# Kernel tuning notes

Hardware: AMD Instinct MI355X
Metric: run time of the kernel (lower is better)

Reference implementation:

```python
import jax, jax.numpy as jnp
import numpy as np

N, E = 10000, 640000
IN_FT, OUT_FT = 512, 128
NEG_SLOPE = 0.2


def setup_inputs() -> dict:
    key = jax.random.key(0)
    ks = jax.random.split(key, 10)
    seq = jax.random.normal(ks[0], (N, IN_FT), dtype=jnp.float32)
    # edges with no self-loops: dst = (src + offset) % N, offset in [1, N-1]
    src = jax.random.randint(ks[1], (E,), 0, N)
    off = jax.random.randint(ks[2], (E,), 1, N)
    dst = (src + off) % N
    edge_index = jnp.stack([src, dst]).astype(jnp.int64)
    # parameters (xavier-ish scale)
    W_fc = jax.random.normal(ks[3], (OUT_FT, IN_FT), dtype=jnp.float32) * (1.0 / np.sqrt(IN_FT))
    W_gat = jax.random.normal(ks[4], (OUT_FT, OUT_FT), dtype=jnp.float32) * (1.0 / np.sqrt(OUT_FT))
    att_src = jax.random.normal(ks[5], (OUT_FT,), dtype=jnp.float32) * 0.1
    att_dst = jax.random.normal(ks[6], (OUT_FT,), dtype=jnp.float32) * 0.1
    gat_bias = jnp.zeros((OUT_FT,), dtype=jnp.float32)
    bias = jnp.zeros((OUT_FT,), dtype=jnp.float32)
    prelu_a = jnp.asarray(0.25, dtype=jnp.float32)
    return {"seq": seq, "edge_index": edge_index, "W_fc": W_fc, "W_gat": W_gat,
            "att_src": att_src, "att_dst": att_dst, "gat_bias": gat_bias,
            "bias": bias, "prelu_a": prelu_a}


def _gat_forward(seq, src, dst, W_fc, W_gat, att_src, att_dst, gat_bias, bias, prelu_a):
    n = seq.shape[0]
    x = seq @ W_fc.T                      # [N, out_ft] fc (no bias)
    h = x @ W_gat.T                       # GATConv internal linear (no bias)
    a_s = h @ att_src                     # [N] per-node src attention logits
    a_d = h @ att_dst                     # [N]
    e = a_s[src] + a_d[dst]               # [E'] per-edge raw score
    e = jnp.where(e >= 0, e, NEG_SLOPE * e)
    # segment softmax over destination node
    m = jax.ops.segment_max(e, dst, num_segments=n)
    m = jnp.where(jnp.isfinite(m), m, 0.0)
    p = jnp.exp(e - m[dst])
    denom = jax.ops.segment_sum(p, dst, num_segments=n)
    alpha = p / (denom[dst] + 1e-16)
    msgs = alpha[:, None] * h[src]        # [E', out_ft]
    out = jax.ops.segment_sum(msgs, dst, num_segments=n) + gat_bias
    out = out + bias
    return jnp.where(out >= 0, out, prelu_a * out)  # PReLU


def reference(seq, edge_index, W_fc, W_gat, att_src, att_dst, gat_bias, bias, prelu_a):
    n = seq.shape[0]
    loops = jnp.arange(n, dtype=edge_index.dtype)   # add_self_loops
    src = jnp.concatenate([edge_index[0], loops])
    dst = jnp.concatenate([edge_index[1], loops])
    return _gat_forward(seq, src, dst, W_fc, W_gat, att_src, att_dst, gat_bias, bias, prelu_a)
```

## Files before the change

kernel.cpp:

```cpp
#include <hip/hip_runtime.h>
#include <hip/hip_bf16.h>

#define IN_FT 512
#define OUT_FT 128
#define NEG_SLOPE 0.2f
#define SHIFT_C 4.0f
#define CAPB 1440
#define NBMAX 1024

typedef __attribute__((ext_vector_type(8))) short short8;
typedef __attribute__((ext_vector_type(4))) short short4v;
typedef __attribute__((ext_vector_type(4))) float float4v;

__device__ inline short f2bf_s(float x) {
    __hip_bfloat16 b = __float2bfloat16(x);
    union { __hip_bfloat16 b; short s; } u;
    u.b = b;
    return u.s;
}
__device__ inline float bf2f(short s) {
    union { float f; unsigned u; } u;
    u.u = ((unsigned)(unsigned short)s) << 16;
    return u.f;
}

__global__ void k_prep(const float* __restrict__ Wg,
                       const float* __restrict__ Wf,
                       short* __restrict__ whf,
                       int* __restrict__ gcur, int nb) {
    if (blockIdx.x >= 256) {
        int i = (blockIdx.x - 256) * 256 + threadIdx.x;
        if (i < nb) gcur[i] = 0;
        return;
    }
    int idx = blockIdx.x * blockDim.x + threadIdx.x;
    int o = idx >> 9;
    int k = idx & 511;
    float s = 0.f;
#pragma unroll 8
    for (int j = 0; j < OUT_FT; ++j)
        s += Wg[o * OUT_FT + j] * Wf[j * IN_FT + k];
    int t = o >> 4, l15 = o & 15;
    int kc = k >> 5, q = (k >> 3) & 3, jj = k & 7;
    whf[(((kc * 8 + t) * 64) + q * 16 + l15) * 8 + jj] = f2bf_s(s);
}

__launch_bounds__(256)
__global__ void k_main(const float* __restrict__ seq,
                       const short8* __restrict__ whf,
                       const float* __restrict__ att_s_v,
                       const float* __restrict__ att_d_v,
                       short* __restrict__ h16,
                       float* __restrict__ a_s,
                       float* __restrict__ a_d,
                       const int* __restrict__ src,
                       const int* __restrict__ dstv,
                       int* __restrict__ gcur,
                       unsigned* __restrict__ bins,
                       int N, int E, int nb, int GB) {
    __shared__ char smem[24576];
    if (blockIdx.x >= GB) {
        int* hist  = (int*)smem;
        int* sbase = hist + NBMAX;
        int* scur  = sbase + NBMAX;
        int e0 = (blockIdx.x - GB) * 2048;
        for (int t = threadIdx.x; t < nb; t += 256) hist[t] = 0;
        __syncthreads();
        int myd[8];
#pragma unroll
        for (int k = 0; k < 8; ++k) {
            int e = e0 + k * 256 + threadIdx.x;
            myd[k] = (e < E) ? dstv[e] : -1;
            if ((unsigned)myd[k] < (unsigned)N) atomicAdd(&hist[myd[k] >> 4], 1);
            else myd[k] = -1;
        }
        __syncthreads();
        for (int t = threadIdx.x; t < nb; t += 256) {
            int c = hist[t];
            sbase[t] = c ? atomicAdd(&gcur[t], c) : 0;
            scur[t] = 0;
        }
        __syncthreads();
#pragma unroll
        for (int k = 0; k < 8; ++k) {
            if (myd[k] >= 0) {
                int e = e0 + k * 256 + threadIdx.x;
                int b = myd[k] >> 4;
                int slot = sbase[b] + atomicAdd(&scur[b], 1);
                if (slot < CAPB) {
                    int s = src[e];
                    if ((unsigned)s >= (unsigned)N) s = 0;
                    bins[(size_t)b * CAPB + slot] = ((unsigned)s << 4) | (myd[k] & 15);
                }
            }
        }
        return;
    }
    short* As = (short*)smem;
    float4v* red = (float4v*)smem;

    int wave = threadIdx.x >> 6;
    int lane = threadIdx.x & 63;
    int l15 = lane & 15, quad = lane >> 4;
    int rows0 = blockIdx.x * 16;

#pragma unroll
    for (int i = 0; i < 8; ++i) {
        int idx = threadIdx.x + 256 * i;
        int r = idx >> 7, c4 = idx & 127;
        int row = rows0 + r;
        int rowc = row < N ? row : N - 1;
        float4 v = *(const float4*)(seq + (size_t)rowc * IN_FT + c4 * 4);
        short4v b;
        b[0] = f2bf_s(v.x); b[1] = f2bf_s(v.y); b[2] = f2bf_s(v.z); b[3] = f2bf_s(v.w);
        int kc = c4 >> 3, q = (c4 >> 1) & 3, half = c4 & 1;
        *(short4v*)(As + (((kc * 4 + q) * 16 + r) * 8 + half * 4)) = b;
    }
    __syncthreads();

    float4v acc[8];
    for (int t = 0; t < 8; ++t) acc[t] = (float4v){0.f, 0.f, 0.f, 0.f};

#pragma unroll
    for (int kk = 0; kk < 4; ++kk) {
        int kc = wave * 4 + kk;
        short8 a = *(const short8*)(As + ((kc * 4 + quad) * 16 + l15) * 8);
        const short8* bhp = whf + (size_t)kc * 512 + lane;
#pragma unroll
        for (int t = 0; t < 8; ++t) {
            short8 bh = bhp[t * 64];
            acc[t] = __builtin_amdgcn_mfma_f32_16x16x32_bf16(a, bh, acc[t], 0, 0, 0);
        }
    }
    __syncthreads();
    if (wave > 0) {
        float4v* base = red + ((wave - 1) * 8) * 64 + lane;
        for (int t = 0; t < 8; ++t) base[t * 64] = acc[t];
    }
    __syncthreads();
    if (wave != 0) return;
    for (int w2 = 0; w2 < 3; ++w2) {
        const float4v* base = red + (w2 * 8) * 64 + lane;
        for (int t = 0; t < 8; ++t) {
            float4v v = base[t * 64];
            acc[t][0] += v[0]; acc[t][1] += v[1]; acc[t][2] += v[2]; acc[t][3] += v[3];
        }
    }
    int rbase = rows0 + quad * 4;
    for (int r = 0; r < 4; ++r) {
        int rr = rbase + r;
        if (rr < N) {
            short* hr = h16 + (size_t)rr * OUT_FT;
            for (int t = 0; t < 8; ++t) hr[t * 16 + l15] = f2bf_s(acc[t][r]);
        }
    }
    float asv[8], adv[8];
    for (int t = 0; t < 8; ++t) {
        asv[t] = att_s_v[t * 16 + l15];
        adv[t] = att_d_v[t * 16 + l15];
    }
    for (int r = 0; r < 4; ++r) {
        float ps = 0.f, pd = 0.f;
        for (int t = 0; t < 8; ++t) {
            float v = acc[t][r];
            ps += v * asv[t];
            pd += v * adv[t];
        }
        for (int m = 1; m < 16; m <<= 1) {
            ps += __shfl_xor(ps, m);
            pd += __shfl_xor(pd, m);
        }
        int rr = rbase + r;
        if (l15 == 0 && rr < N) { a_s[rr] = ps; a_d[rr] = pd; }
    }
}

__launch_bounds__(256)
__global__ void k_agg(const short* __restrict__ h16, const float* __restrict__ a_s,
                      const float* __restrict__ a_d,
                      const int* __restrict__ gcur, const unsigned* __restrict__ bins,
                      const float* __restrict__ gat_bias,
                      const float* __restrict__ bias,
                      const float* __restrict__ prelu_a,
                      float* __restrict__ out, int N) {
    __shared__ int   srcs[CAPB];
    __shared__ float pvals[CAPB];
    __shared__ int   hist[16], base[16], cur16[16];
    __shared__ float ads[16];
    int b = blockIdx.x;
    int d0 = b << 4;
    int nd = N - d0; if (nd > 16) nd = 16;
    int tid = threadIdx.x;

    if (tid < 16) {
        hist[tid] = 0;
        ads[tid] = (tid < nd) ? a_d[d0 + tid] : 0.f;
    }
    __syncthreads();

    int cnt = gcur[b]; if (cnt > CAPB) cnt = CAPB;
    const unsigned* binp = bins + (size_t)b * CAPB;

    for (int c = tid; c < cnt; c += 256) atomicAdd(&hist[binp[c] & 15], 1);
    __syncthreads();
    if (tid == 0) {
        int run = 0;
        for (int i = 0; i < 16; ++i) { base[i] = run; run += hist[i]; cur16[i] = 0; }
    }
    __syncthreads();
    for (int c = tid; c < cnt; c += 256) {
        unsigned pk = binp[c];
        int dl = pk & 15, sv = pk >> 4;
        float ev = a_s[sv] + ads[dl];
        ev = (ev >= 0.f) ? ev : NEG_SLOPE * ev;
        float p = __expf(ev - SHIFT_C);
        int slot = base[dl] + atomicAdd(&cur16[dl], 1);
        srcs[slot] = sv;
        pvals[slot] = p;
    }
    __syncthreads();

    int w = tid >> 6, L = tid & 63;
    float b0 = gat_bias[2 * L] + bias[2 * L];
    float b1 = gat_bias[2 * L + 1] + bias[2 * L + 1];
    float pa = prelu_a[0];
    for (int dl = w; dl < nd; dl += 4) {
        int d = d0 + dl;
        float adi = ads[dl];
        float e0 = a_s[d] + adi;
        e0 = (e0 >= 0.f) ? e0 : NEG_SLOPE * e0;
        float p0 = __expf(e0 - SHIFT_C);
        short2 hs0 = *(const short2*)(h16 + (size_t)d * OUT_FT + 2 * L);
        float acc0 = p0 * bf2f(hs0.x), acc1 = p0 * bf2f(hs0.y);
        float dsum = 0.f;
        int beg = base[dl], n = hist[dl];
        for (int c = 0; c < n; c += 64) {
            int nv = n - c; if (nv > 64) nv = 64;
            int sv = 0; float pl = 0.f;
            if (L < nv) { sv = srcs[beg + c + L]; pl = pvals[beg + c + L]; }
            dsum += pl;
            int e = 0;
            for (; e + 16 <= nv; e += 16) {
#pragma unroll
                for (int k = 0; k < 16; ++k) {
                    float p = __shfl(pl, e + k);
                    int ss = __shfl(sv, e + k);
                    short2 hv = *(const short2*)(h16 + (size_t)ss * OUT_FT + 2 * L);
                    acc0 += p * bf2f(hv.x);
                    acc1 += p * bf2f(hv.y);
                }
            }
            for (; e < nv; ++e) {
                float p = __shfl(pl, e);
                int ss = __shfl(sv, e);
                short2 hv = *(const short2*)(h16 + (size_t)ss * OUT_FT + 2 * L);
                acc0 += p * bf2f(hv.x);
                acc1 += p * bf2f(hv.y);
            }
        }
        for (int m = 1; m < 64; m <<= 1) dsum += __shfl_xor(dsum, m);
        float inv = 1.f / (dsum + p0 + 1e-16f);
        float o0 = acc0 * inv + b0;
        float o1 = acc1 * inv + b1;
        o0 = (o0 >= 0.f) ? o0 : pa * o0;
        o1 = (o1 >= 0.f) ? o1 : pa * o1;
        float2 ov; ov.x = o0; ov.y = o1;
        *(float2*)(out + (size_t)d * OUT_FT + 2 * L) = ov;
    }
}

extern "C" void kernel_launch(void* const* d_in, const int* in_sizes, int n_in,
                              void* d_out, int out_size, void* d_ws, size_t ws_size,
                              hipStream_t stream) {
    const float* seq     = (const float*)d_in[0];
    const int*   ei      = (const int*)d_in[1];
    const float* W_fc    = (const float*)d_in[2];
    const float* W_gat   = (const float*)d_in[3];
    const float* att_src = (const float*)d_in[4];
    const float* att_dst = (const float*)d_in[5];
    const float* gat_b   = (const float*)d_in[6];
    const float* bias    = (const float*)d_in[7];
    const float* prelu_a = (const float*)d_in[8];

    int N = in_sizes[0] / IN_FT;
    int E = in_sizes[1] / 2;
    const int* src = ei;
    const int* dst = ei + E;
    int nb = (N + 15) >> 4;

    char* wsb = (char*)d_ws;
    size_t cur = 0;
    auto alloc = [&](size_t bytes) -> void* {
        void* p = (void*)(wsb + cur);
        cur += (bytes + 255) & ~(size_t)255;
        return p;
    };
    short*    h16  = (short*)alloc((size_t)N * OUT_FT * 2);
    float*    a_s  = (float*)alloc((size_t)N * 4);
    float*    a_d  = (float*)alloc((size_t)N * 4);
    int*      gcur = (int*)alloc((size_t)nb * 4);
    unsigned* bins = (unsigned*)alloc((size_t)nb * CAPB * 4);
    short*    whf  = (short*)alloc((size_t)OUT_FT * IN_FT * 2);

    int GB = (N + 15) / 16;
    int PB = (E + 2047) / 2048;

    k_prep<<<dim3(256 + (nb + 255) / 256), dim3(256), 0, stream>>>(W_gat, W_fc, whf, gcur, nb);
    k_main<<<dim3(GB + PB), dim3(256), 0, stream>>>(
        seq, (const short8*)whf, att_src, att_dst, h16, a_s, a_d,
        src, dst, gcur, bins, N, E, nb, GB);
    k_agg<<<dim3(nb), dim3(256), 0, stream>>>(
        h16, a_s, a_d, gcur, bins, gat_b, bias, prelu_a, (float*)d_out, N);
}
```

Measured before the change: 139.3 us.

## Shrink aggregation buckets to 8 destinations and gather h rows without shuffles

Destination buckets go from 16 to 8 nodes. That doubles the number of aggregation blocks and halves the shared-memory footprint per block. Sources and weights are packed into one int2 LDS array, and the inner loop reads them as a broadcast from LDS instead of using wave shuffles. The loop batches 8 gathers of h16 rows before accumulating, to expose memory-level parallelism. The gcur zeroing moves from an extra k_prep block range to hipMemsetAsync, which adds one stream operation.

```diff
diff --git a/kernel.cpp b/kernel.cpp
--- a/kernel.cpp
+++ b/kernel.cpp
@@ -5,8 +5,8 @@
 #define OUT_FT 128
 #define NEG_SLOPE 0.2f
 #define SHIFT_C 4.0f
-#define CAPB 1440
-#define NBMAX 1024
+#define CAP8 768
+#define NBMAX 1280
 
 typedef __attribute__((ext_vector_type(8))) short short8;
 typedef __attribute__((ext_vector_type(4))) short short4v;
@@ -26,13 +26,7 @@
 
 __global__ void k_prep(const float* __restrict__ Wg,
                        const float* __restrict__ Wf,
-                       short* __restrict__ whf,
-                       int* __restrict__ gcur, int nb) {
-    if (blockIdx.x >= 256) {
-        int i = (blockIdx.x - 256) * 256 + threadIdx.x;
-        if (i < nb) gcur[i] = 0;
-        return;
-    }
+                       short* __restrict__ whf) {
     int idx = blockIdx.x * blockDim.x + threadIdx.x;
     int o = idx >> 9;
     int k = idx & 511;
@@ -71,7 +65,7 @@
         for (int k = 0; k < 8; ++k) {
             int e = e0 + k * 256 + threadIdx.x;
             myd[k] = (e < E) ? dstv[e] : -1;
-            if ((unsigned)myd[k] < (unsigned)N) atomicAdd(&hist[myd[k] >> 4], 1);
+            if ((unsigned)myd[k] < (unsigned)N) atomicAdd(&hist[myd[k] >> 3], 1);
             else myd[k] = -1;
         }
         __syncthreads();
@@ -85,12 +79,12 @@
         for (int k = 0; k < 8; ++k) {
             if (myd[k] >= 0) {
                 int e = e0 + k * 256 + threadIdx.x;
-                int b = myd[k] >> 4;
+                int b = myd[k] >> 3;
                 int slot = sbase[b] + atomicAdd(&scur[b], 1);
-                if (slot < CAPB) {
+                if (slot < CAP8) {
                     int s = src[e];
                     if ((unsigned)s >= (unsigned)N) s = 0;
-                    bins[(size_t)b * CAPB + slot] = ((unsigned)s << 4) | (myd[k] & 15);
+                    bins[(size_t)b * CAP8 + slot] = ((unsigned)s << 3) | (myd[k] & 7);
                 }
             }
         }
@@ -183,40 +177,39 @@
                       const float* __restrict__ bias,
                       const float* __restrict__ prelu_a,
                       float* __restrict__ out, int N) {
-    __shared__ int   srcs[CAPB];
-    __shared__ float pvals[CAPB];
-    __shared__ int   hist[16], base[16], cur16[16];
-    __shared__ float ads[16];
+    __shared__ int2  spair[CAP8];
+    __shared__ int   hist[8], base[8], cur8[8];
+    __shared__ float ads[8];
     int b = blockIdx.x;
-    int d0 = b << 4;
-    int nd = N - d0; if (nd > 16) nd = 16;
+    int d0 = b << 3;
+    int nd = N - d0; if (nd > 8) nd = 8;
     int tid = threadIdx.x;
 
-    if (tid < 16) {
+    if (tid < 8) {
         hist[tid] = 0;
         ads[tid] = (tid < nd) ? a_d[d0 + tid] : 0.f;
     }
     __syncthreads();
 
-    int cnt = gcur[b]; if (cnt > CAPB) cnt = CAPB;
-    const unsigned* binp = bins + (size_t)b * CAPB;
-
-    for (int c = tid; c < cnt; c += 256) atomicAdd(&hist[binp[c] & 15], 1);
+    int cnt = gcur[b]; if (cnt > CAP8) cnt = CAP8;
+    const unsigned* binp = bins + (size_t)b * CAP8;
+
+    for (int c = tid; c < cnt; c += 256) atomicAdd(&hist[binp[c] & 7], 1);
     __syncthreads();
     if (tid == 0) {
         int run = 0;
-        for (int i = 0; i < 16; ++i) { base[i] = run; run += hist[i]; cur16[i] = 0; }
+        for (int i = 0; i < 8; ++i) { base[i] = run; run += hist[i]; cur8[i] = 0; }
     }
     __syncthreads();
     for (int c = tid; c < cnt; c += 256) {
         unsigned pk = binp[c];
-        int dl = pk & 15, sv = pk >> 4;
+        int dl = pk & 7, sv = pk >> 3;
         float ev = a_s[sv] + ads[dl];
         ev = (ev >= 0.f) ? ev : NEG_SLOPE * ev;
         float p = __expf(ev - SHIFT_C);
-        int slot = base[dl] + atomicAdd(&cur16[dl], 1);
-        srcs[slot] = sv;
-        pvals[slot] = p;
+        int slot = base[dl] + atomicAdd(&cur8[dl], 1);
+        int2 sp; sp.x = sv; sp.y = __float_as_int(p);
+        spair[slot] = sp;
     }
     __syncthreads();
 
@@ -234,31 +227,30 @@
         float acc0 = p0 * bf2f(hs0.x), acc1 = p0 * bf2f(hs0.y);
         float dsum = 0.f;
         int beg = base[dl], n = hist[dl];
-        for (int c = 0; c < n; c += 64) {
-            int nv = n - c; if (nv > 64) nv = 64;
-            int sv = 0; float pl = 0.f;
-            if (L < nv) { sv = srcs[beg + c + L]; pl = pvals[beg + c + L]; }
-            dsum += pl;
-            int e = 0;
-            for (; e + 16 <= nv; e += 16) {
-#pragma unroll
-                for (int k = 0; k < 16; ++k) {
-                    float p = __shfl(pl, e + k);
-                    int ss = __shfl(sv, e + k);
-                    short2 hv = *(const short2*)(h16 + (size_t)ss * OUT_FT + 2 * L);
-                    acc0 += p * bf2f(hv.x);
-                    acc1 += p * bf2f(hv.y);
-                }
+        int e = 0;
+        for (; e + 8 <= n; e += 8) {
+            float pp[8]; short2 hh[8];
+#pragma unroll
+            for (int j = 0; j < 8; ++j) {
+                int2 sp = spair[beg + e + j];
+                pp[j] = __int_as_float(sp.y);
+                hh[j] = *(const short2*)(h16 + (size_t)sp.x * OUT_FT + 2 * L);
             }
-            for (; e < nv; ++e) {
-                float p = __shfl(pl, e);
-                int ss = __shfl(sv, e);
-                short2 hv = *(const short2*)(h16 + (size_t)ss * OUT_FT + 2 * L);
-                acc0 += p * bf2f(hv.x);
-                acc1 += p * bf2f(hv.y);
+#pragma unroll
+            for (int j = 0; j < 8; ++j) {
+                dsum += pp[j];
+                acc0 += pp[j] * bf2f(hh[j].x);
+                acc1 += pp[j] * bf2f(hh[j].y);
             }
         }
-        for (int m = 1; m < 64; m <<= 1) dsum += __shfl_xor(dsum, m);
+        for (; e < n; ++e) {
+            int2 sp = spair[beg + e];
+            float p = __int_as_float(sp.y);
+            short2 hv = *(const short2*)(h16 + (size_t)sp.x * OUT_FT + 2 * L);
+            dsum += p;
+            acc0 += p * bf2f(hv.x);
+            acc1 += p * bf2f(hv.y);
+        }
         float inv = 1.f / (dsum + p0 + 1e-16f);
         float o0 = acc0 * inv + b0;
         float o1 = acc1 * inv + b1;
@@ -286,7 +278,7 @@
     int E = in_sizes[1] / 2;
     const int* src = ei;
     const int* dst = ei + E;
-    int nb = (N + 15) >> 4;
+    int nb = (N + 7) >> 3;
 
     char* wsb = (char*)d_ws;
     size_t cur = 0;
@@ -299,13 +291,14 @@
     float*    a_s  = (float*)alloc((size_t)N * 4);
     float*    a_d  = (float*)alloc((size_t)N * 4);
     int*      gcur = (int*)alloc((size_t)nb * 4);
-    unsigned* bins = (unsigned*)alloc((size_t)nb * CAPB * 4);
+    unsigned* bins = (unsigned*)alloc((size_t)nb * CAP8 * 4);
     short*    whf  = (short*)alloc((size_t)OUT_FT * IN_FT * 2);
 
     int GB = (N + 15) / 16;
     int PB = (E + 2047) / 2048;
 
-    k_prep<<<dim3(256 + (nb + 255) / 256), dim3(256), 0, stream>>>(W_gat, W_fc, whf, gcur, nb);
+    hipMemsetAsync(gcur, 0, (size_t)nb * 4, stream);
+    k_prep<<<dim3(256), dim3(256), 0, stream>>>(W_gat, W_fc, whf);
     k_main<<<dim3(GB + PB), dim3(256), 0, stream>>>(
         seq, (const short8*)whf, att_src, att_dst, h16, a_s, a_d,
         src, dst, gcur, bins, N, E, nb, GB);
```

Measured after the change: 131.4 us. 5.7% less time.
